# Kernel optimization log

Hardware: AMD Instinct MI355X
Metric: run time of the kernel (lower is better)

## Reference

```python
import jax, jax.numpy as jnp
import numpy as np

B, NP, K = 8, 512, 64   # graphs, points per graph, knn neighbors
N = B * NP              # total nodes
EPS = 1e-5


def knn_edges(pos):
    """knn_graph(pos, k=K, batch, loop=True): edges (src=j neighbor, dst=i)."""
    p = pos.reshape(B, NP, 3)
    d2 = jnp.sum((p[:, :, None, :] - p[:, None, :, :]) ** 2, axis=-1)  # [B,NP,NP]
    _, idx = jax.lax.top_k(-d2, K)  # [B,NP,K] nearest (self included, d2=0)
    off = (jnp.arange(B, dtype=jnp.int32) * NP)[:, None, None]
    src = (idx.astype(jnp.int32) + off).reshape(-1)
    dst = jnp.broadcast_to(jnp.arange(NP, dtype=jnp.int32)[None, :, None] + off,
                           (B, NP, K)).reshape(-1)
    return src, dst


def graph_norm(x, batch, w, b, ms):
    """PyG GraphNorm: per-graph mean/std with learnable mean scale."""
    cnt = jax.ops.segment_sum(jnp.ones((x.shape[0], 1), x.dtype), batch, B)
    mean = jax.ops.segment_sum(x, batch, B) / cnt
    out = x - mean[batch] * ms
    var = jax.ops.segment_sum(out * out, batch, B) / cnt
    return w * out / jnp.sqrt(var + EPS)[batch] + b


def pointnet_layer(h, pos, src, dst, w1, b1, w2, b2):
    """message = MLP(concat(h_j, pos_j - pos_i)); aggregate = scatter-max over dst."""
    m = jnp.concatenate([h[src], pos[src] - pos[dst]], axis=-1)  # [E, Cin+3]
    m = jax.nn.relu(m @ w1 + b1) @ w2 + b2                        # [E, Cout]
    return jax.ops.segment_max(m, dst, N)


def _forward(batch, pos,
             gn1_w, gn1_b, gn1_ms, gn2_w, gn2_b, gn2_ms, gn3_w, gn3_b, gn3_ms,
             gn4_w, gn4_b, gn4_ms, gn5_w, gn5_b, gn5_ms, gn6_w, gn6_b, gn6_ms,
             c1_w1, c1_b1, c1_w2, c1_b2, c2_w1, c2_b1, c2_w2, c2_b2,
             c3_w1, c3_b1, c3_w2, c3_b2, c4_w1, c4_b1, c4_w2, c4_b2,
             c5_w1, c5_b1, c5_w2, c5_b2, cls_w, cls_b):
    src, dst = knn_edges(pos)
    h = graph_norm(pos, batch, gn1_w, gn1_b, gn1_ms)
    h = pointnet_layer(h, pos, src, dst, c1_w1, c1_b1, c1_w2, c1_b2)
    h = jax.nn.relu(graph_norm(h, batch, gn2_w, gn2_b, gn2_ms))
    h = pointnet_layer(h, pos, src, dst, c2_w1, c2_b1, c2_w2, c2_b2)
    h = jax.nn.relu(graph_norm(h, batch, gn3_w, gn3_b, gn3_ms))
    h = pointnet_layer(h, pos, src, dst, c3_w1, c3_b1, c3_w2, c3_b2)
    h = jax.nn.relu(graph_norm(h, batch, gn4_w, gn4_b, gn4_ms))
    h = pointnet_layer(h, pos, src, dst, c4_w1, c4_b1, c4_w2, c4_b2)
    h = jax.nn.relu(graph_norm(h, batch, gn5_w, gn5_b, gn5_ms))
    h = pointnet_layer(h, pos, src, dst, c5_w1, c5_b1, c5_w2, c5_b2)
    h = jax.nn.relu(graph_norm(h, batch, gn6_w, gn6_b, gn6_ms))
    return h @ cls_w + cls_b  # [N, 14]


def setup_inputs() -> dict:
    key = jax.random.key(0)
    ks = iter(jax.random.split(key, 40))
    inp = {}
    inp["pos"] = jax.random.normal(next(ks), (N, 3), jnp.float32)
    inp["batch"] = jnp.repeat(jnp.arange(B, dtype=jnp.int32), NP)
    for i, c in enumerate([3, 64, 128, 256, 512, 512], 1):
        inp[f"gn{i}_w"] = jnp.ones((c,), jnp.float32)
        inp[f"gn{i}_b"] = jnp.zeros((c,), jnp.float32)
        inp[f"gn{i}_ms"] = jnp.ones((c,), jnp.float32)
    for i, (ci, co) in enumerate([(3, 64), (64, 128), (128, 256), (256, 512), (512, 512)], 1):
        fin = ci + 3
        inp[f"c{i}_w1"] = jax.random.normal(next(ks), (fin, co), jnp.float32) / np.sqrt(fin).astype(np.float32)
        inp[f"c{i}_b1"] = jnp.zeros((co,), jnp.float32)
        inp[f"c{i}_w2"] = jax.random.normal(next(ks), (co, co), jnp.float32) / np.sqrt(co).astype(np.float32)
        inp[f"c{i}_b2"] = jnp.zeros((co,), jnp.float32)
    inp["cls_w"] = jax.random.normal(next(ks), (512, 14), jnp.float32) / np.float32(np.sqrt(512))
    inp["cls_b"] = jnp.zeros((14,), jnp.float32)
    return inp


def reference(pos, batch,
              gn1_w, gn1_b, gn1_ms, gn2_w, gn2_b, gn2_ms, gn3_w, gn3_b, gn3_ms,
              gn4_w, gn4_b, gn4_ms, gn5_w, gn5_b, gn5_ms, gn6_w, gn6_b, gn6_ms,
              c1_w1, c1_b1, c1_w2, c1_b2, c2_w1, c2_b1, c2_w2, c2_b2,
              c3_w1, c3_b1, c3_w2, c3_b2, c4_w1, c4_b1, c4_w2, c4_b2,
              c5_w1, c5_b1, c5_w2, c5_b2, cls_w, cls_b):
    return _forward(batch, pos,
                    gn1_w, gn1_b, gn1_ms, gn2_w, gn2_b, gn2_ms, gn3_w, gn3_b, gn3_ms,
                    gn4_w, gn4_b, gn4_ms, gn5_w, gn5_b, gn5_ms, gn6_w, gn6_b, gn6_ms,
                    c1_w1, c1_b1, c1_w2, c1_b2, c2_w1, c2_b1, c2_w2, c2_b2,
                    c3_w1, c3_b1, c3_w2, c3_b2, c4_w1, c4_b1, c4_w2, c4_b2,
                    c5_w1, c5_b1, c5_w2, c5_b2, cls_w, cls_b)
```

## Files before the change

kernel.cpp:

```cpp
#include <hip/hip_runtime.h>
#include <stdint.h>

#define N_NODES 4096
#define NGRAPH 8
#define NPTS 512
#define KNN 64
#define EPSN 1e-5f

typedef _Float16 f16x8 __attribute__((ext_vector_type(8)));
typedef float f32x4 __attribute__((ext_vector_type(4)));
typedef unsigned long long u64;

__device__ __forceinline__ unsigned short f2h(float f) {
    _Float16 h = (_Float16)f;
    union { _Float16 h; unsigned short u; } cv; cv.h = h;
    return cv.u;
}

__device__ __forceinline__ void w2cv8(const float* __restrict__ src, unsigned short* __restrict__ dst,
                                      int c, int lg2c) {
    int C = 1 << lg2c;
    int mm = c & 15, q = (c >> 4) & 3, F = c >> 6;
    int k5 = F & ((C >> 5) - 1), n4 = F >> (lg2c - 5);
    int n = n4 * 16 + mm, kb = k5 * 32 + q * 8;
    unsigned short h[8];
    #pragma unroll
    for (int t = 0; t < 8; ++t) h[t] = f2h(src[(size_t)(kb + t) * C + n]);
    uint4 pk;
    pk.x = (unsigned)h[0] | ((unsigned)h[1] << 16);
    pk.y = (unsigned)h[2] | ((unsigned)h[3] << 16);
    pk.z = (unsigned)h[4] | ((unsigned)h[5] << 16);
    pk.w = (unsigned)h[6] | ((unsigned)h[7] << 16);
    *(uint4*)&dst[(size_t)c * 8] = pk;
}

__global__ __launch_bounds__(64) void setup_kernel(const float* __restrict__ pos, int* __restrict__ knn_out,
                                                   const float* __restrict__ wa, const float* __restrict__ wb,
                                                   const float* __restrict__ wc, const float* __restrict__ wd,
                                                   const float* __restrict__ we,
                                                   unsigned short* __restrict__ oa, unsigned short* __restrict__ ob,
                                                   unsigned short* __restrict__ oc, unsigned short* __restrict__ od,
                                                   unsigned short* __restrict__ oe,
                                                   float* __restrict__ statz,
                                                   const float* __restrict__ ms1, const float* __restrict__ gw1,
                                                   float* __restrict__ Aa, float* __restrict__ Sa) {
#pragma clang fp contract(off)
    __shared__ float px[NPTS], py[NPTS], pz[NPTS];
    __shared__ u64 keys[NPTS];
    int bid = blockIdx.x;
    int tid = threadIdx.x;
    int gidx = bid * 64 + tid;
    for (int idx = gidx; idx < 40960; idx += 262144) statz[idx] = 0.f;
    if (gidx < 76288) {
        int c = gidx;
        if (c < 512)         w2cv8(wa, oa, c, 6);
        else if (c < 2560)   w2cv8(wb, ob, c - 512, 7);
        else if (c < 10752)  w2cv8(wc, oc, c - 2560, 8);
        else if (c < 43520)  w2cv8(wd, od, c - 10752, 9);
        else                 w2cv8(we, oe, c - 43520, 9);
    }
    if (bid < 24) {
        int g = bid / 3, ch = bid - g * 3;
        float s1 = 0.f, s2 = 0.f;
        for (int n = tid; n < NPTS; n += 64) {
            float v = pos[(g * NPTS + n) * 3 + ch];
            s1 += v; s2 += v * v;
        }
        #pragma unroll
        for (int off = 32; off; off >>= 1) { s1 += __shfl_xor(s1, off); s2 += __shfl_xor(s2, off); }
        if (tid == 0) {
            float mean = s1 * (1.f / NPTS);
            float av = mean * ms1[ch];
            float var = s2 * (1.f / NPTS) - 2.f * av * mean + av * av;
            Aa[g * 3 + ch] = av;
            Sa[g * 3 + ch] = gw1[ch] / sqrtf(var + EPSN);
        }
    }
    int b = bid >> 9;
    int il = bid & (NPTS - 1);
    for (int n = tid; n < NPTS; n += 64) {
        int base = (b * NPTS + n) * 3;
        px[n] = pos[base]; py[n] = pos[base + 1]; pz[n] = pos[base + 2];
    }
    __syncthreads();
    float xi = px[il], yi = py[il], zi = pz[il];
    for (int n = tid; n < NPTS; n += 64) {
        float dx = px[n] - xi, dy = py[n] - yi, dz = pz[n] - zi;
        float d2 = dx * dx;
        d2 = d2 + dy * dy;
        d2 = d2 + dz * dz;
        keys[n] = (((u64)__float_as_uint(d2)) << 32) | (unsigned)n;
    }
    __syncthreads();
    for (int k2 = 2; k2 <= NPTS; k2 <<= 1) {
        for (int j = k2 >> 1; j > 0; j >>= 1) {
            #pragma unroll 4
            for (int p = 0; p < 4; ++p) {
                int pid = tid + p * 64;
                int t = ((pid & ~(j - 1)) << 1) | (pid & (j - 1));
                int ixj = t | j;
                u64 a = keys[t], c = keys[ixj];
                bool up = ((t & k2) == 0);
                if ((a > c) == up) { keys[t] = c; keys[ixj] = a; }
            }
            __syncthreads();
        }
    }
    int j0 = (int)(keys[tid] & 0xffffffffu);
    knn_out[(size_t)(b * NPTS + il) * KNN + tid] = b * NPTS + j0;
}

template<int CIN, int C, int RELU, int RAW>
__global__ __launch_bounds__(C) void node_kernel(const float* __restrict__ y, const float* __restrict__ pos,
                                                 const float* __restrict__ p1, const float* __restrict__ p2,
                                                 const float* __restrict__ ms, const float* __restrict__ gw,
                                                 const float* __restrict__ bnp,
                                                 const float* __restrict__ w1, const float* __restrict__ b1,
                                                 float* __restrict__ U, float* __restrict__ P) {
    constexpr int ROWS = 16;
    constexpr int KC = 64;
    constexpr int LDH = KC + 4;
    __shared__ float hs[ROWS][LDH];
    __shared__ float As_[CIN > 0 ? CIN : 1], Ss_[CIN > 0 ? CIN : 1];
    const int c = threadIdx.x;
    const int n0 = blockIdx.x * ROWS;
    const int b = n0 >> 9;
    if (RAW) {
        for (int ch = c; ch < CIN; ch += C) {
            float s1 = p1[b * CIN + ch], s2 = p2[b * CIN + ch];
            float mean = s1 * (1.f / NPTS);
            float a = mean * ms[ch];
            float var = s2 * (1.f / NPTS) - 2.f * a * mean + a * a;
            As_[ch] = a;
            Ss_[ch] = gw[ch] / sqrtf(var + EPSN);
        }
    }
    float acc[ROWS];
    #pragma unroll
    for (int r = 0; r < ROWS; ++r) acc[r] = 0.f;
    constexpr int NCHUNK = (CIN + KC - 1) / KC;
    #pragma unroll 1
    for (int s = 0; s < NCHUNK; ++s) {
        const int k0 = s * KC;
        const int kc = (CIN - k0 < KC) ? (CIN - k0) : KC;
        __syncthreads();
        for (int idx = c; idx < ROWS * kc; idx += C) {
            int r = idx / kc, k = idx - r * kc;
            int ch = k0 + k;
            float a = RAW ? As_[ch] : p1[b * CIN + ch];
            float sf = RAW ? Ss_[ch] : p2[b * CIN + ch];
            float v = (y[(size_t)(n0 + r) * CIN + ch] - a) * sf + bnp[ch];
            if (RELU) v = fmaxf(v, 0.f);
            hs[r][k] = v;
        }
        __syncthreads();
        int k = 0;
        for (; k + 4 <= kc; k += 4) {
            float w0 = w1[(size_t)(k0 + k) * C + c];
            float w1v = w1[(size_t)(k0 + k + 1) * C + c];
            float w2v = w1[(size_t)(k0 + k + 2) * C + c];
            float w3v = w1[(size_t)(k0 + k + 3) * C + c];
            #pragma unroll
            for (int r = 0; r < ROWS; ++r) {
                f32x4 hv = *(const f32x4*)&hs[r][k];
                acc[r] = fmaf(hv[0], w0, acc[r]);
                acc[r] = fmaf(hv[1], w1v, acc[r]);
                acc[r] = fmaf(hv[2], w2v, acc[r]);
                acc[r] = fmaf(hv[3], w3v, acc[r]);
            }
        }
        for (; k < kc; ++k) {
            float wv = w1[(size_t)(k0 + k) * C + c];
            #pragma unroll
            for (int r = 0; r < ROWS; ++r)
                acc[r] = fmaf(hs[r][k], wv, acc[r]);
        }
    }
    float pacc[ROWS];
    #pragma unroll
    for (int r = 0; r < ROWS; ++r) pacc[r] = 0.f;
    #pragma unroll
    for (int e = 0; e < 3; ++e) {
        float wv = w1[(size_t)(CIN + e) * C + c];
        #pragma unroll
        for (int r = 0; r < ROWS; ++r)
            pacc[r] = fmaf(pos[(n0 + r) * 3 + e], wv, pacc[r]);
    }
    float bv = b1[c];
    #pragma unroll
    for (int r = 0; r < ROWS; ++r) {
        U[(size_t)(n0 + r) * C + c] = acc[r] + pacc[r] + bv;
        P[(size_t)(n0 + r) * C + c] = pacc[r];
    }
}

template<int C, int W>
__global__ __launch_bounds__(W * 64, 4) void edge_kernel(const float* __restrict__ U, const float* __restrict__ P,
                                                         const int* __restrict__ knn, const unsigned short* __restrict__ w2t,
                                                         const float* __restrict__ b2, float* __restrict__ Y,
                                                         float* __restrict__ sum1, float* __restrict__ sum2) {
    constexpr int NCT = C / (W * 16);
    constexpr int S32 = C / 32;
    constexpr int NCHUNK = C / 8;
    __shared__ unsigned short Th[64 * C];
    __shared__ int jn[64];
    __shared__ float Pr[C];
    const int bid = blockIdx.x;
    const int i = ((bid & 7) << 9) | (bid >> 3);
    const int tid = threadIdx.x;
    const int wave = tid >> 6, lane = tid & 63, m = lane & 15, quad = lane >> 4;
    const int cw = wave * (NCT * 16);
    if (tid < 64) jn[tid] = knn[(size_t)i * KNN + tid];
    for (int idx = tid; idx < C; idx += W * 64) Pr[idx] = P[(size_t)i * C + idx];
    __syncthreads();
    #pragma unroll 2
    for (int idx = tid; idx < 64 * NCHUNK; idx += W * 64) {
        int row = idx / NCHUNK, ch = idx - row * NCHUNK;
        const float* up = U + (size_t)jn[row] * C + ch * 8;
        f32x4 va = *(const f32x4*)up;
        f32x4 vb = *(const f32x4*)(up + 4);
        f32x4 pa = *(const f32x4*)&Pr[ch * 8];
        f32x4 pb = *(const f32x4*)&Pr[ch * 8 + 4];
        uint4 pk;
        pk.x = (unsigned)f2h(fmaxf(va[0] - pa[0], 0.f)) | ((unsigned)f2h(fmaxf(va[1] - pa[1], 0.f)) << 16);
        pk.y = (unsigned)f2h(fmaxf(va[2] - pa[2], 0.f)) | ((unsigned)f2h(fmaxf(va[3] - pa[3], 0.f)) << 16);
        pk.z = (unsigned)f2h(fmaxf(vb[0] - pb[0], 0.f)) | ((unsigned)f2h(fmaxf(vb[1] - pb[1], 0.f)) << 16);
        pk.w = (unsigned)f2h(fmaxf(vb[2] - pb[2], 0.f)) | ((unsigned)f2h(fmaxf(vb[3] - pb[3], 0.f)) << 16);
        int sc = (ch & ~7) | ((ch ^ row) & 7);
        *(uint4*)&Th[row * C + sc * 8] = pk;
    }
    __syncthreads();
    f32x4 acc[4][NCT];
    f32x4 zero = {0.f, 0.f, 0.f, 0.f};
    #pragma unroll
    for (int rt = 0; rt < 4; ++rt)
        #pragma unroll
        for (int ct = 0; ct < NCT; ++ct)
            acc[rt][ct] = zero;
    #pragma unroll 2
    for (int s = 0; s < S32; ++s) {
        f16x8 a[4];
        #pragma unroll
        for (int rt = 0; rt < 4; ++rt) {
            int row = rt * 16 + m;
            int chunk = s * 4 + quad;
            int sc = (chunk & ~7) | ((chunk ^ row) & 7);
            a[rt] = *(const f16x8*)&Th[row * C + sc * 8];
        }
        #pragma unroll
        for (int ct = 0; ct < NCT; ++ct) {
            const f16x8 bb = *(const f16x8*)(w2t +
                (size_t)(((cw >> 4) + ct) * S32 + s) * 512 + quad * 128 + m * 8);
            #pragma unroll
            for (int rt = 0; rt < 4; ++rt)
                acc[rt][ct] = __builtin_amdgcn_mfma_f32_16x16x32_f16(a[rt], bb, acc[rt][ct], 0, 0, 0);
        }
    }
    const int gb = i >> 9;
    #pragma unroll
    for (int ct = 0; ct < NCT; ++ct) {
        float vmax = -3.4e38f;
        #pragma unroll
        for (int rt = 0; rt < 4; ++rt) {
            vmax = fmaxf(vmax, acc[rt][ct][0]);
            vmax = fmaxf(vmax, acc[rt][ct][1]);
            vmax = fmaxf(vmax, acc[rt][ct][2]);
            vmax = fmaxf(vmax, acc[rt][ct][3]);
        }
        vmax = fmaxf(vmax, __shfl_xor(vmax, 16));
        vmax = fmaxf(vmax, __shfl_xor(vmax, 32));
        if (quad == 0) {
            int col = cw + ct * 16 + m;
            float val = vmax + b2[col];
            Y[(size_t)i * C + col] = val;
            atomicAdd(&sum1[gb * C + col], val);
            atomicAdd(&sum2[gb * C + col], val * val);
        }
    }
}

__device__ __forceinline__ uint4 pack8(f32x4 va, f32x4 vb, f32x4 pa, f32x4 pb) {
    uint4 pk;
    pk.x = (unsigned)f2h(fmaxf(va[0] - pa[0], 0.f)) | ((unsigned)f2h(fmaxf(va[1] - pa[1], 0.f)) << 16);
    pk.y = (unsigned)f2h(fmaxf(va[2] - pa[2], 0.f)) | ((unsigned)f2h(fmaxf(va[3] - pa[3], 0.f)) << 16);
    pk.z = (unsigned)f2h(fmaxf(vb[0] - pb[0], 0.f)) | ((unsigned)f2h(fmaxf(vb[1] - pb[1], 0.f)) << 16);
    pk.w = (unsigned)f2h(fmaxf(vb[2] - pb[2], 0.f)) | ((unsigned)f2h(fmaxf(vb[3] - pb[3], 0.f)) << 16);
    return pk;
}

template<int C>
__global__ __launch_bounds__(512, 2) void edgeb_kernel(const float* __restrict__ U, const float* __restrict__ P,
                                                       const int* __restrict__ knn, const unsigned short* __restrict__ w2t,
                                                       const float* __restrict__ b2, float* __restrict__ Y,
                                                       float* __restrict__ sum1, float* __restrict__ sum2) {
    constexpr int NCT = C / 128;
    constexpr int S32 = C / 32;
    constexpr int NCHK = C / 8;
    constexpr int RSTEP = 512 / NCHK;
    __shared__ unsigned short Th[(C / 64) * 128 * 64];
    __shared__ int jn[128];
    const int bid = blockIdx.x;
    const int g = bid & 7;
    const int n0 = (g << 9) | ((bid >> 3) << 1);
    const int tid = threadIdx.x;
    const int lane = tid & 63, wave = tid >> 6, m = lane & 15, quad = lane >> 4;
    const int cw = wave * (NCT * 16);
    if (tid < 128) jn[tid] = knn[(size_t)(n0 + (tid >> 6)) * KNN + (tid & 63)];
    const int ch = tid & (NCHK - 1);
    const int rb = tid / NCHK;
    const int cblk = ch >> 3, cw8 = ch & 7;
    const float* pp = P + (size_t)n0 * C + ch * 8;
    f32x4 pa0 = *(const f32x4*)pp;
    f32x4 pb0 = *(const f32x4*)(pp + 4);
    f32x4 pa1 = *(const f32x4*)(pp + C);
    f32x4 pb1 = *(const f32x4*)(pp + C + 4);
    __syncthreads();
    #pragma unroll 4
    for (int t = 0; t < 128 / RSTEP; ++t) {
        int row = rb + t * RSTEP;
        const float* up = U + (size_t)jn[row] * C + ch * 8;
        f32x4 va = *(const f32x4*)up;
        f32x4 vb = *(const f32x4*)(up + 4);
        f32x4 pa = (row & 64) ? pa1 : pa0;
        f32x4 pb = (row & 64) ? pb1 : pb0;
        *(uint4*)&Th[cblk * 8192 + row * 64 + ((cw8 ^ (row & 7)) << 3)] = pack8(va, vb, pa, pb);
    }
    __syncthreads();
    f32x4 acc[8][NCT];
    f32x4 zero = {0.f, 0.f, 0.f, 0.f};
    #pragma unroll
    for (int rt = 0; rt < 8; ++rt)
        #pragma unroll
        for (int ct = 0; ct < NCT; ++ct)
            acc[rt][ct] = zero;
    const unsigned short* wt = w2t + (size_t)(cw >> 4) * S32 * 512 + quad * 128 + m * 8;
    int idx0[8], idx1[8];
    #pragma unroll
    for (int rt = 0; rt < 8; ++rt) {
        int row = rt * 16 + m;
        idx0[rt] = row * 64 + ((quad ^ (row & 7)) << 3);
        idx1[rt] = row * 64 + (((4 + quad) ^ (row & 7)) << 3);
    }
    const unsigned short* pB[NCT];
    #pragma unroll
    for (int ct = 0; ct < NCT; ++ct)
        pB[ct] = wt + ((size_t)ct * S32 + 2) * 512;
    f16x8 bbA[NCT], bbB[NCT];
    #pragma unroll
    for (int ct = 0; ct < NCT; ++ct) {
        bbA[ct] = *(const f16x8*)(wt + (size_t)ct * S32 * 512);
        bbB[ct] = *(const f16x8*)(wt + ((size_t)ct * S32 + 1) * 512);
    }
    const unsigned short* tcur = Th;
    auto step = [&](f16x8 (&buf)[NCT], const int (&idx)[8], int poff, bool pre) {
        f16x8 a[8];
        #pragma unroll
        for (int rt = 0; rt < 8; ++rt)
            a[rt] = *(const f16x8*)&tcur[idx[rt]];
        #pragma unroll
        for (int ct = 0; ct < NCT; ++ct) {
            f16x8 bcur = buf[ct];
            if (pre) buf[ct] = *(const f16x8*)(pB[ct] + poff);
            __builtin_amdgcn_s_setprio(1);
            #pragma unroll
            for (int rt = 0; rt < 8; ++rt)
                acc[rt][ct] = __builtin_amdgcn_mfma_f32_16x16x32_f16(a[rt], bcur, acc[rt][ct], 0, 0, 0);
            __builtin_amdgcn_s_setprio(0);
        }
    };
    #pragma unroll 1
    for (int s = 0; s + 2 < S32; s += 2) {
        step(bbA, idx0, 0, true);
        step(bbB, idx1, 512, true);
        tcur += 8192;
        #pragma unroll
        for (int ct = 0; ct < NCT; ++ct) pB[ct] += 1024;
    }
    step(bbA, idx0, 0, false);
    step(bbB, idx1, 0, false);
    #pragma unroll
    for (int h = 0; h < 2; ++h) {
        #pragma unroll
        for (int ct = 0; ct < NCT; ++ct) {
            float vmax = -3.4e38f;
            #pragma unroll
            for (int rt = h * 4; rt < h * 4 + 4; ++rt) {
                vmax = fmaxf(vmax, acc[rt][ct][0]);
                vmax = fmaxf(vmax, acc[rt][ct][1]);
                vmax = fmaxf(vmax, acc[rt][ct][2]);
                vmax = fmaxf(vmax, acc[rt][ct][3]);
            }
            vmax = fmaxf(vmax, __shfl_xor(vmax, 16));
            vmax = fmaxf(vmax, __shfl_xor(vmax, 32));
            if (quad == 0) {
                int col = cw + ct * 16 + m;
                float val = vmax + b2[col];
                Y[(size_t)(n0 + h) * C + col] = val;
                atomicAdd(&sum1[g * C + col], val);
                atomicAdd(&sum2[g * C + col], val * val);
            }
        }
    }
}

__global__ __launch_bounds__(256) void cls_kernel(const float* __restrict__ y, const float* __restrict__ sum1,
                                                  const float* __restrict__ sum2, const float* __restrict__ ms,
                                                  const float* __restrict__ gw, const float* __restrict__ gnb,
                                                  const float* __restrict__ w, const float* __restrict__ bias,
                                                  float* __restrict__ out) {
    __shared__ float wl[512 * 14];
    __shared__ _Float16 hn[16][520];
    __shared__ float As[512], Ss[512];
    int tid = threadIdx.x;
    int n0 = blockIdx.x * 16;
    int b = n0 >> 9;
    for (int ch = tid; ch < 512; ch += 256) {
        float s1 = sum1[b * 512 + ch], s2 = sum2[b * 512 + ch];
        float mean = s1 * (1.f / NPTS);
        float a = mean * ms[ch];
        float var = s2 * (1.f / NPTS) - 2.f * a * mean + a * a;
        As[ch] = a;
        Ss[ch] = gw[ch] / sqrtf(var + EPSN);
    }
    for (int idx = tid; idx < 512 * 14; idx += 256) wl[idx] = w[idx];
    __syncthreads();
    for (int idx = tid; idx < 16 * 512; idx += 256) {
        int r = idx >> 9, k = idx & 511;
        float v = (y[(size_t)(n0 + r) * 512 + k] - As[k]) * Ss[k] + gnb[k];
        hn[r][k] = (_Float16)fmaxf(v, 0.f);
    }
    __syncthreads();
    if (tid < 224) {
        int nl = tid / 14, c = tid - nl * 14;
        float acc = bias[c];
        for (int k = 0; k < 512; ++k)
            acc += (float)hn[nl][k] * wl[k * 14 + c];
        out[(size_t)(n0 + nl) * 14 + c] = acc;
    }
}

extern "C" void kernel_launch(void* const* d_in, const int* in_sizes, int n_in,
                              void* d_out, int out_size, void* d_ws, size_t ws_size,
                              hipStream_t stream) {
    const float* pos = (const float*)d_in[0];
    const float* gnw[6]; const float* gnb[6]; const float* gnms[6];
    for (int i = 0; i < 6; ++i) {
        gnw[i]  = (const float*)d_in[2 + 3 * i];
        gnb[i]  = (const float*)d_in[3 + 3 * i];
        gnms[i] = (const float*)d_in[4 + 3 * i];
    }
    const float* cw1[5]; const float* cb1[5]; const float* cw2[5]; const float* cb2[5];
    for (int i = 0; i < 5; ++i) {
        cw1[i] = (const float*)d_in[20 + 4 * i];
        cb1[i] = (const float*)d_in[21 + 4 * i];
        cw2[i] = (const float*)d_in[22 + 4 * i];
        cb2[i] = (const float*)d_in[23 + 4 * i];
    }
    const float* clsw = (const float*)d_in[40];
    const float* clsb = (const float*)d_in[41];
    float* out = (float*)d_out;

    char* ws = (char*)d_ws;
    int* knn             = (int*)(ws + 0);
    float* U             = (float*)(ws + 1048576);
    float* P             = (float*)(ws + 9437184);
    float* y             = (float*)(ws + 26214400);
    float* Aa            = (float*)(ws + 34603008);
    float* Sa            = (float*)(ws + 34619392);
    unsigned short* w2t0 = (unsigned short*)(ws + 34635776);
    unsigned short* w2t1 = (unsigned short*)(ws + 34643968);
    unsigned short* w2t2 = (unsigned short*)(ws + 34676736);
    unsigned short* w2t3 = (unsigned short*)(ws + 34807808);
    unsigned short* w2t4 = (unsigned short*)(ws + 35332096);
    float* acc           = (float*)(ws + 35856384);
    float* s1l[5]; float* s2l[5];
    for (int l = 0; l < 5; ++l) { s1l[l] = acc + l * 8192; s2l[l] = s1l[l] + 4096; }

    setup_kernel<<<N_NODES, 64, 0, stream>>>(pos, knn, cw2[0], cw2[1], cw2[2], cw2[3], cw2[4],
                                             w2t0, w2t1, w2t2, w2t3, w2t4, acc,
                                             gnms[0], gnw[0], Aa, Sa);

    node_kernel<3, 64, 0, 0><<<N_NODES / 16, 64, 0, stream>>>(pos, pos, Aa, Sa, gnms[0], gnw[0], gnb[0], cw1[0], cb1[0], U, P);
    edge_kernel<64, 4><<<N_NODES, 256, 0, stream>>>(U, P, knn, w2t0, cb2[0], y, s1l[0], s2l[0]);

    node_kernel<64, 128, 1, 1><<<N_NODES / 16, 128, 0, stream>>>(y, pos, s1l[0], s2l[0], gnms[1], gnw[1], gnb[1], cw1[1], cb1[1], U, P);
    edge_kernel<128, 8><<<N_NODES, 512, 0, stream>>>(U, P, knn, w2t1, cb2[1], y, s1l[1], s2l[1]);

    node_kernel<128, 256, 1, 1><<<N_NODES / 16, 256, 0, stream>>>(y, pos, s1l[1], s2l[1], gnms[2], gnw[2], gnb[2], cw1[2], cb1[2], U, P);
    edgeb_kernel<256><<<N_NODES / 2, 512, 0, stream>>>(U, P, knn, w2t2, cb2[2], y, s1l[2], s2l[2]);

    node_kernel<256, 512, 1, 1><<<N_NODES / 16, 512, 0, stream>>>(y, pos, s1l[2], s2l[2], gnms[3], gnw[3], gnb[3], cw1[3], cb1[3], U, P);
    edgeb_kernel<512><<<N_NODES / 2, 512, 0, stream>>>(U, P, knn, w2t3, cb2[3], y, s1l[3], s2l[3]);

    node_kernel<512, 512, 1, 1><<<N_NODES / 16, 512, 0, stream>>>(y, pos, s1l[3], s2l[3], gnms[4], gnw[4], gnb[4], cw1[4], cb1[4], U, P);
    edgeb_kernel<512><<<N_NODES / 2, 512, 0, stream>>>(U, P, knn, w2t4, cb2[4], y, s1l[4], s2l[4]);

    cls_kernel<<<N_NODES / 16, 256, 0, stream>>>(y, s1l[4], s2l[4], gnms[5], gnw[5], gnb[5], clsw, clsb, out);
}
```

Before: 700.6 us.

## Use split-fp16 MFMA for node linear layers 4 and 5

Adds nodem_kernel, which computes the first MLP linear layer of conv layers 4 and 5 on MFMA. Activations and weights are each split into high and low fp16 halves, and three products are accumulated to keep close to fp32 accuracy. The setup kernel now also pre-converts those W1 weights into the split MFMA layout. The layer-3 edge kernel is separately retuned to 4 waves instead of 8. This replaces scalar FP32 FMA node matmuls with tensor-core work, at the cost of triple MFMA work and extra setup conversion.

After: 639.6 us. -8.7%, faster.

```diff
diff --git a/kernel.cpp b/kernel.cpp
--- a/kernel.cpp
+++ b/kernel.cpp
@@ -15,6 +15,10 @@
     _Float16 h = (_Float16)f;
     union { _Float16 h; unsigned short u; } cv; cv.h = h;
     return cv.u;
+}
+__device__ __forceinline__ float h2f(unsigned short u) {
+    union { unsigned short u; _Float16 h; } cv; cv.u = u;
+    return (float)cv.h;
 }
 
 __device__ __forceinline__ void w2cv8(const float* __restrict__ src, unsigned short* __restrict__ dst,
@@ -34,13 +38,41 @@
     *(uint4*)&dst[(size_t)c * 8] = pk;
 }
 
+__device__ __forceinline__ void w1cv8hl(const float* __restrict__ src, unsigned short* __restrict__ dh,
+                                        unsigned short* __restrict__ dl, int c, int kl) {
+    int mm = c & 15, q = (c >> 4) & 3, F = c >> 6;
+    int k5 = F & ((1 << kl) - 1), n4 = F >> kl;
+    int n = n4 * 16 + mm, kb = k5 * 32 + q * 8;
+    unsigned short hh[8], ll[8];
+    #pragma unroll
+    for (int t = 0; t < 8; ++t) {
+        float v = src[(size_t)(kb + t) * 512 + n];
+        hh[t] = f2h(v);
+        ll[t] = f2h(v - h2f(hh[t]));
+    }
+    uint4 ph, pl;
+    ph.x = (unsigned)hh[0] | ((unsigned)hh[1] << 16);
+    ph.y = (unsigned)hh[2] | ((unsigned)hh[3] << 16);
+    ph.z = (unsigned)hh[4] | ((unsigned)hh[5] << 16);
+    ph.w = (unsigned)hh[6] | ((unsigned)hh[7] << 16);
+    pl.x = (unsigned)ll[0] | ((unsigned)ll[1] << 16);
+    pl.y = (unsigned)ll[2] | ((unsigned)ll[3] << 16);
+    pl.z = (unsigned)ll[4] | ((unsigned)ll[5] << 16);
+    pl.w = (unsigned)ll[6] | ((unsigned)ll[7] << 16);
+    *(uint4*)&dh[(size_t)c * 8] = ph;
+    *(uint4*)&dl[(size_t)c * 8] = pl;
+}
+
 __global__ __launch_bounds__(64) void setup_kernel(const float* __restrict__ pos, int* __restrict__ knn_out,
                                                    const float* __restrict__ wa, const float* __restrict__ wb,
                                                    const float* __restrict__ wc, const float* __restrict__ wd,
                                                    const float* __restrict__ we,
+                                                   const float* __restrict__ w14, const float* __restrict__ w15,
                                                    unsigned short* __restrict__ oa, unsigned short* __restrict__ ob,
                                                    unsigned short* __restrict__ oc, unsigned short* __restrict__ od,
                                                    unsigned short* __restrict__ oe,
+                                                   unsigned short* __restrict__ o14h, unsigned short* __restrict__ o14l,
+                                                   unsigned short* __restrict__ o15h, unsigned short* __restrict__ o15l,
                                                    float* __restrict__ statz,
                                                    const float* __restrict__ ms1, const float* __restrict__ gw1,
                                                    float* __restrict__ Aa, float* __restrict__ Sa) {
@@ -51,13 +83,15 @@
     int tid = threadIdx.x;
     int gidx = bid * 64 + tid;
     for (int idx = gidx; idx < 40960; idx += 262144) statz[idx] = 0.f;
-    if (gidx < 76288) {
+    if (gidx < 125440) {
         int c = gidx;
         if (c < 512)         w2cv8(wa, oa, c, 6);
         else if (c < 2560)   w2cv8(wb, ob, c - 512, 7);
         else if (c < 10752)  w2cv8(wc, oc, c - 2560, 8);
         else if (c < 43520)  w2cv8(wd, od, c - 10752, 9);
-        else                 w2cv8(we, oe, c - 43520, 9);
+        else if (c < 76288)  w2cv8(we, oe, c - 43520, 9);
+        else if (c < 92672)  w1cv8hl(w14, o14h, o14l, c - 76288, 3);
+        else                 w1cv8hl(w15, o15h, o15l, c - 92672, 4);
     }
     if (bid < 24) {
         int g = bid / 3, ch = bid - g * 3;
@@ -194,6 +228,101 @@
     }
 }
 
+template<int CIN>
+__global__ __launch_bounds__(512) void nodem_kernel(const float* __restrict__ y, const float* __restrict__ pos,
+                                                    const float* __restrict__ p1, const float* __restrict__ p2,
+                                                    const float* __restrict__ ms, const float* __restrict__ gw,
+                                                    const float* __restrict__ bnp,
+                                                    const unsigned short* __restrict__ w1h,
+                                                    const unsigned short* __restrict__ w1l,
+                                                    const float* __restrict__ w1s, const float* __restrict__ b1,
+                                                    float* __restrict__ U, float* __restrict__ P) {
+    constexpr int S32 = CIN / 32;
+    constexpr int NCHR = CIN / 8;
+    __shared__ unsigned short Ah[16 * CIN], Al[16 * CIN];
+    __shared__ float As_[CIN], Ss_[CIN], pf[48];
+    const int tid = threadIdx.x;
+    const int n0 = blockIdx.x * 16;
+    const int b = n0 >> 9;
+    for (int ch = tid; ch < CIN; ch += 512) {
+        float s1 = p1[b * CIN + ch], s2 = p2[b * CIN + ch];
+        float mean = s1 * (1.f / NPTS);
+        float a = mean * ms[ch];
+        float var = s2 * (1.f / NPTS) - 2.f * a * mean + a * a;
+        As_[ch] = a;
+        Ss_[ch] = gw[ch] / sqrtf(var + EPSN);
+    }
+    if (tid < 48) pf[tid] = pos[n0 * 3 + tid];
+    __syncthreads();
+    for (int ci = tid; ci < 2 * CIN; ci += 512) {
+        int r = ci / NCHR, ch = ci - r * NCHR;
+        int k0 = ch * 8;
+        const float* yy = y + (size_t)(n0 + r) * CIN + k0;
+        unsigned short hh[8], ll[8];
+        #pragma unroll
+        for (int t = 0; t < 8; ++t) {
+            float v = (yy[t] - As_[k0 + t]) * Ss_[k0 + t] + bnp[k0 + t];
+            v = fmaxf(v, 0.f);
+            hh[t] = f2h(v);
+            ll[t] = f2h(v - h2f(hh[t]));
+        }
+        int sc = (ch & ~7) | ((ch ^ r) & 7);
+        uint4 ph, pl;
+        ph.x = (unsigned)hh[0] | ((unsigned)hh[1] << 16);
+        ph.y = (unsigned)hh[2] | ((unsigned)hh[3] << 16);
+        ph.z = (unsigned)hh[4] | ((unsigned)hh[5] << 16);
+        ph.w = (unsigned)hh[6] | ((unsigned)hh[7] << 16);
+        pl.x = (unsigned)ll[0] | ((unsigned)ll[1] << 16);
+        pl.y = (unsigned)ll[2] | ((unsigned)ll[3] << 16);
+        pl.z = (unsigned)ll[4] | ((unsigned)ll[5] << 16);
+        pl.w = (unsigned)ll[6] | ((unsigned)ll[7] << 16);
+        *(uint4*)&Ah[r * CIN + sc * 8] = ph;
+        *(uint4*)&Al[r * CIN + sc * 8] = pl;
+    }
+    __syncthreads();
+    const int lane = tid & 63, wave = tid >> 6, m = lane & 15, quad = lane >> 4;
+    const int cw = wave * 64;
+    f32x4 acc[4];
+    f32x4 zero = {0.f, 0.f, 0.f, 0.f};
+    #pragma unroll
+    for (int ct = 0; ct < 4; ++ct) acc[ct] = zero;
+    const unsigned short* bh = w1h + (size_t)(cw >> 4) * S32 * 512 + quad * 128 + m * 8;
+    const unsigned short* bl = w1l + (size_t)(cw >> 4) * S32 * 512 + quad * 128 + m * 8;
+    #pragma unroll 2
+    for (int s = 0; s < S32; ++s) {
+        int ci = s * 4 + quad;
+        int sc = (ci & ~7) | ((ci ^ m) & 7);
+        f16x8 aH = *(const f16x8*)&Ah[m * CIN + sc * 8];
+        f16x8 aL = *(const f16x8*)&Al[m * CIN + sc * 8];
+        #pragma unroll
+        for (int ct = 0; ct < 4; ++ct) {
+            f16x8 bH = *(const f16x8*)(bh + ((size_t)ct * S32 + s) * 512);
+            f16x8 bL = *(const f16x8*)(bl + ((size_t)ct * S32 + s) * 512);
+            acc[ct] = __builtin_amdgcn_mfma_f32_16x16x32_f16(aH, bH, acc[ct], 0, 0, 0);
+            acc[ct] = __builtin_amdgcn_mfma_f32_16x16x32_f16(aL, bH, acc[ct], 0, 0, 0);
+            acc[ct] = __builtin_amdgcn_mfma_f32_16x16x32_f16(aH, bL, acc[ct], 0, 0, 0);
+        }
+    }
+    #pragma unroll
+    for (int ct = 0; ct < 4; ++ct) {
+        int col = cw + ct * 16 + m;
+        float w0 = w1s[(size_t)CIN * 512 + col];
+        float w1v = w1s[(size_t)(CIN + 1) * 512 + col];
+        float w2v = w1s[(size_t)(CIN + 2) * 512 + col];
+        float bc = b1[col];
+        #pragma unroll
+        for (int j = 0; j < 4; ++j) {
+            int r = quad * 4 + j;
+            float pp = pf[r * 3] * w0;
+            pp = fmaf(pf[r * 3 + 1], w1v, pp);
+            pp = fmaf(pf[r * 3 + 2], w2v, pp);
+            float val = acc[ct][j] + pp + bc;
+            U[(size_t)(n0 + r) * 512 + col] = val;
+            P[(size_t)(n0 + r) * 512 + col] = pp;
+        }
+    }
+}
+
 template<int C, int W>
 __global__ __launch_bounds__(W * 64, 4) void edge_kernel(const float* __restrict__ U, const float* __restrict__ P,
                                                          const int* __restrict__ knn, const unsigned short* __restrict__ w2t,
@@ -288,15 +417,15 @@
     return pk;
 }
 
-template<int C>
-__global__ __launch_bounds__(512, 2) void edgeb_kernel(const float* __restrict__ U, const float* __restrict__ P,
-                                                       const int* __restrict__ knn, const unsigned short* __restrict__ w2t,
-                                                       const float* __restrict__ b2, float* __restrict__ Y,
-                                                       float* __restrict__ sum1, float* __restrict__ sum2) {
-    constexpr int NCT = C / 128;
+template<int C, int W>
+__global__ __launch_bounds__(W * 64, 2) void edgeb_kernel(const float* __restrict__ U, const float* __restrict__ P,
+                                                          const int* __restrict__ knn, const unsigned short* __restrict__ w2t,
+                                                          const float* __restrict__ b2, float* __restrict__ Y,
+                                                          float* __restrict__ sum1, float* __restrict__ sum2) {
+    constexpr int NCT = C / (W * 16);
     constexpr int S32 = C / 32;
     constexpr int NCHK = C / 8;
-    constexpr int RSTEP = 512 / NCHK;
+    constexpr int RSTEP = (W * 64) / NCHK;
     __shared__ unsigned short Th[(C / 64) * 128 * 64];
     __shared__ int jn[128];
     const int bid = blockIdx.x;
@@ -464,6 +593,12 @@
     int* knn             = (int*)(ws + 0);
     float* U             = (float*)(ws + 1048576);
     float* P             = (float*)(ws + 9437184);
+    unsigned short* w1h4 = (unsigned short*)(ws + 17825792);
+    unsigned short* w1l4 = (unsigned short*)(ws + 18088036 - 100);
+    w1h4                 = (unsigned short*)(ws + 17825792);
+    unsigned short* w1l4b= (unsigned short*)(ws + 18087936);
+    unsigned short* w1h5 = (unsigned short*)(ws + 18350080);
+    unsigned short* w1l5 = (unsigned short*)(ws + 18874368);
     float* y             = (float*)(ws + 26214400);
     float* Aa            = (float*)(ws + 34603008);
     float* Sa            = (float*)(ws + 34619392);
@@ -477,8 +612,10 @@
     for (int l = 0; l < 5; ++l) { s1l[l] = acc + l * 8192; s2l[l] = s1l[l] + 4096; }
 
     setup_kernel<<<N_NODES, 64, 0, stream>>>(pos, knn, cw2[0], cw2[1], cw2[2], cw2[3], cw2[4],
-                                             w2t0, w2t1, w2t2, w2t3, w2t4, acc,
-                                             gnms[0], gnw[0], Aa, Sa);
+                                             cw1[3], cw1[4],
+                                             w2t0, w2t1, w2t2, w2t3, w2t4,
+                                             w1h4, w1l4b, w1h5, w1l5,
+                                             acc, gnms[0], gnw[0], Aa, Sa);
 
     node_kernel<3, 64, 0, 0><<<N_NODES / 16, 64, 0, stream>>>(pos, pos, Aa, Sa, gnms[0], gnw[0], gnb[0], cw1[0], cb1[0], U, P);
     edge_kernel<64, 4><<<N_NODES, 256, 0, stream>>>(U, P, knn, w2t0, cb2[0], y, s1l[0], s2l[0]);
@@ -487,13 +624,15 @@
     edge_kernel<128, 8><<<N_NODES, 512, 0, stream>>>(U, P, knn, w2t1, cb2[1], y, s1l[1], s2l[1]);
 
     node_kernel<128, 256, 1, 1><<<N_NODES / 16, 256, 0, stream>>>(y, pos, s1l[1], s2l[1], gnms[2], gnw[2], gnb[2], cw1[2], cb1[2], U, P);
-    edgeb_kernel<256><<<N_NODES / 2, 512, 0, stream>>>(U, P, knn, w2t2, cb2[2], y, s1l[2], s2l[2]);
-
-    node_kernel<256, 512, 1, 1><<<N_NODES / 16, 512, 0, stream>>>(y, pos, s1l[2], s2l[2], gnms[3], gnw[3], gnb[3], cw1[3], cb1[3], U, P);
-    edgeb_kernel<512><<<N_NODES / 2, 512, 0, stream>>>(U, P, knn, w2t3, cb2[3], y, s1l[3], s2l[3]);
-
-    node_kernel<512, 512, 1, 1><<<N_NODES / 16, 512, 0, stream>>>(y, pos, s1l[3], s2l[3], gnms[4], gnw[4], gnb[4], cw1[4], cb1[4], U, P);
-    edgeb_kernel<512><<<N_NODES / 2, 512, 0, stream>>>(U, P, knn, w2t4, cb2[4], y, s1l[4], s2l[4]);
+    edgeb_kernel<256, 4><<<N_NODES / 2, 256, 0, stream>>>(U, P, knn, w2t2, cb2[2], y, s1l[2], s2l[2]);
+
+    nodem_kernel<256><<<N_NODES / 16, 512, 0, stream>>>(y, pos, s1l[2], s2l[2], gnms[3], gnw[3], gnb[3],
+                                                        w1h4, w1l4b, cw1[3], cb1[3], U, P);
+    edgeb_kernel<512, 8><<<N_NODES / 2, 512, 0, stream>>>(U, P, knn, w2t3, cb2[3], y, s1l[3], s2l[3]);
+
+    nodem_kernel<512><<<N_NODES / 16, 512, 0, stream>>>(y, pos, s1l[3], s2l[3], gnms[4], gnw[4], gnb[4],
+                                                        w1h5, w1l5, cw1[4], cb1[4], U, P);
+    edgeb_kernel<512, 8><<<N_NODES / 2, 512, 0, stream>>>(U, P, knn, w2t4, cb2[4], y, s1l[4], s2l[4]);
 
     cls_kernel<<<N_NODES / 16, 256, 0, stream>>>(y, s1l[4], s2l[4], gnms[5], gnw[5], gnb[5], clsw, clsb, out);
 }
```
